# Performance work log

Hardware: AMD Instinct MI355X
Metric: run time of the kernel (lower is better)

The kernel has to match this reference:

```python
import jax, jax.numpy as jnp
import numpy as np

KNOTS = 8
INTERVAL = 4.0
LAYERS = 8
WIDTH = 128
DX = 64
DY = 64
P = 3 * KNOTS - 1  # widths(K) + heights(K) + interior derivatives(K-1)
BATCH = 16384
MIN_DERIV = 1e-3
SOFTMAX_ADJ = 1e-2


def _made_masks(D, W):
    in_deg = np.arange(1, D + 1)
    hid_deg = (np.arange(W) % max(D - 1, 1)) + 1
    m1 = (hid_deg[:, None] >= in_deg[None, :]).astype(np.float32)        # (W, D)
    out_deg = np.repeat(np.arange(1, D + 1), P)                           # (D*P,)
    m2 = (out_deg[:, None] > hid_deg[None, :]).astype(np.float32)        # (D*P, W)
    return jnp.asarray(m1), jnp.asarray(m2)


def _adj_softmax(v):
    p = jax.nn.softmax(v, axis=-1)
    return (p + SOFTMAX_ADJ / v.shape[-1]) / (1.0 + SOFTMAX_ADJ)


def _rqs_transform(x, params):
    # x: (B, D); params: (B, D, P). Rational-quadratic spline on [-B_int, B_int], identity outside.
    Bi = INTERVAL
    w = params[..., :KNOTS]
    h = params[..., KNOTS:2 * KNOTS]
    d = params[..., 2 * KNOTS:]
    widths = _adj_softmax(w) * 2 * Bi
    heights = _adj_softmax(h) * 2 * Bi
    zero = jnp.zeros(x.shape + (1,), x.dtype)
    x_pos = -Bi + jnp.concatenate([zero, jnp.cumsum(widths, -1)], -1)   # (B, D, K+1)
    y_pos = -Bi + jnp.concatenate([zero, jnp.cumsum(heights, -1)], -1)
    derivs = jax.nn.softplus(d) + MIN_DERIV                              # (B, D, K-1)
    one = jnp.ones(x.shape + (1,), x.dtype)
    derivs = jnp.concatenate([one, derivs, one], -1)                     # (B, D, K+1), boundary derivs = 1
    inside = (x > -Bi) & (x < Bi)
    xc = jnp.clip(x, -Bi, Bi)
    # bin search (K is small; vectorized comparison)
    k = jnp.clip(jnp.sum((xc[..., None] >= x_pos), -1) - 1, 0, KNOTS - 1)

    def g(a, i):
        return jnp.take_along_axis(a, i[..., None], -1)[..., 0]

    xk, xk1 = g(x_pos, k), g(x_pos, k + 1)
    yk, yk1 = g(y_pos, k), g(y_pos, k + 1)
    dk, dk1 = g(derivs, k), g(derivs, k + 1)
    sk = (yk1 - yk) / (xk1 - xk)
    xi = (xc - xk) / (xk1 - xk)
    omx = 1.0 - xi
    den = sk + (dk1 + dk - 2.0 * sk) * xi * omx
    out = yk + (yk1 - yk) * (sk * xi * xi + dk * xi * omx) / den
    ld = 2.0 * jnp.log(sk) + jnp.log(dk1 * xi * xi + 2.0 * sk * xi * omx + dk * omx * omx) - 2.0 * jnp.log(den)
    return jnp.where(inside, out, x), jnp.where(inside, ld, 0.0)


def _maf_transform(x, W1, b1, Wout, bout, D):
    # Stacked layers: masked MLP -> elementwise RQ spline -> reverse permutation.
    m1, m2 = _made_masks(D, WIDTH)

    def layer(carry, ws):
        xc, ld = carry
        w1, bb1, wo, bo = ws
        hdn = jax.nn.relu(xc @ (w1 * m1).T + bb1)                # (B, W)
        p = (hdn @ (wo * m2).T + bo).reshape(xc.shape[0], D, P)  # (B, D, P)
        x2, ldj = _rqs_transform(xc, p)
        return (x2[:, ::-1], ld + ldj.sum(-1)), None

    init = (x, jnp.zeros(x.shape[0], x.dtype))
    (xf, ld), _ = jax.lax.scan(layer, init, (W1, b1, Wout, bout))
    return xf, ld


def setup_inputs() -> dict:
    key = jax.random.key(0)
    ks = jax.random.split(key, 10)
    s = 0.05
    return {
        "x": jax.random.normal(ks[0], (BATCH, DX), jnp.float32),
        "y": jax.random.normal(ks[1], (BATCH, DY), jnp.float32),
        "f_W1": jax.random.normal(ks[2], (LAYERS, WIDTH, DX), jnp.float32) * s,
        "f_b1": jnp.zeros((LAYERS, WIDTH), jnp.float32),
        "f_Wout": jax.random.normal(ks[3], (LAYERS, DX * P, WIDTH), jnp.float32) * s,
        "f_bout": jnp.zeros((LAYERS, DX * P), jnp.float32),
        "g_W1": jax.random.normal(ks[4], (LAYERS, WIDTH, DY), jnp.float32) * s,
        "g_b1": jnp.zeros((LAYERS, WIDTH), jnp.float32),
        "g_Wout": jax.random.normal(ks[5], (LAYERS, DY * P, WIDTH), jnp.float32) * s,
        "g_bout": jnp.zeros((LAYERS, DY * P), jnp.float32),
    }


def reference(x, y, f_W1, f_b1, f_Wout, f_bout, g_W1, g_b1, g_Wout, g_bout):
    xo, ldf = _maf_transform(x, f_W1, f_b1, f_Wout, f_bout, DX)
    yo, ldg = _maf_transform(y, g_W1, g_b1, g_Wout, g_bout, DY)
    return (xo, ldf, yo, ldg)
```

## Files before the change

kernel.cpp:

```cpp
#include <hip/hip_runtime.h>
#include <math.h>

#define BATCH   16384
#define DIMS    64
#define WID     128
#define KN      8
#define NP      23
#define NCOL    (DIMS * NP)
#define NLAYERS 8
#define BI_F    4.0f
#define GRP     92
#define NGRP    16
#define XPITCH  68
#define PCP     104
#define LOG2E   1.44269504f

#define PF_WOUT (NLAYERS * NCOL * WID)
#define PF_W1   (NLAYERS * WID * DIMS)

typedef short s16x8 __attribute__((ext_vector_type(8)));
typedef unsigned short u16x8 __attribute__((ext_vector_type(8)));
typedef float f32x4 __attribute__((ext_vector_type(4)));

__device__ __forceinline__ unsigned short f2bf(float f) {
    unsigned int u = __builtin_bit_cast(unsigned int, f);
    unsigned int r = (u + 0x7FFFu + ((u >> 16) & 1u)) >> 16;
    return (unsigned short)r;
}
__device__ __forceinline__ float bfLO(unsigned int u) {
    return __builtin_bit_cast(float, u << 16);
}
__device__ __forceinline__ float bfHI(unsigned int u) {
    return __builtin_bit_cast(float, u & 0xffff0000u);
}
__device__ __forceinline__ unsigned int cvtpk_bf16(float a, float b) {
    unsigned int r;
    asm("v_cvt_pk_bf16_f32 %0, %1, %2" : "=v"(r) : "v"(a), "v"(b));
    return r;
}

__device__ __forceinline__ void stage16(const unsigned short* g, unsigned short* l) {
    __builtin_amdgcn_global_load_lds(
        (__attribute__((address_space(1))) void*)g,
        (__attribute__((address_space(3))) void*)l,
        16, 0, 0);
}

__global__ __launch_bounds__(256) void premask_kernel(
    const float* __restrict__ f_wout, const float* __restrict__ g_wout,
    const float* __restrict__ f_w1,   const float* __restrict__ g_w1,
    unsigned short* __restrict__ womask, unsigned short* __restrict__ w1mask)
{
    const int idx    = blockIdx.x * 256 + threadIdx.x;
    const int stride = gridDim.x * 256;

    const int totw = 2 * PF_WOUT;
    for (int i = idx; i < totw; i += stride) {
        int fl = i / PF_WOUT;
        int r  = i % PF_WOUT;
        int h  = r % WID;
        int o  = (r / WID) % NCOL;
        int d  = o / NP;
        int hd = h % (DIMS - 1) + 1;
        const float* src = fl ? g_wout : f_wout;
        unsigned short v = (hd <= d) ? f2bf(src[r] * LOG2E) : (unsigned short)0;
        const int dst = i - h + (h ^ ((o & 7) << 4));
        womask[dst] = v;
    }

    const int tot1 = 2 * PF_W1;
    for (int i = idx; i < tot1; i += stride) {
        int fl = i / PF_W1;
        int r  = i % PF_W1;
        int c  = r % DIMS;
        int w  = (r / DIMS) % WID;
        int deg = w % (DIMS - 1) + 1;
        const float* src = fl ? g_w1 : f_w1;
        w1mask[i] = (c < deg) ? f2bf(src[r]) : (unsigned short)0;
    }
}

__global__ __launch_bounds__(256)
__attribute__((amdgpu_waves_per_eu(2, 2)))
void flow8_kernel(
    const float* __restrict__ xin_f, const float* __restrict__ xin_g,
    float* __restrict__ xout_f,      float* __restrict__ xout_g,
    const unsigned short* __restrict__ w1m_f, const unsigned short* __restrict__ w1m_g,
    const float* __restrict__ b1_f,  const float* __restrict__ b1_g,
    const unsigned short* __restrict__ wom_f, const unsigned short* __restrict__ wom_g,
    const float* __restrict__ bo_f,  const float* __restrict__ bo_g,
    float* __restrict__ ld_f,        float* __restrict__ ld_g)
{
    __shared__ __align__(16) unsigned short Wl[GRP * WID];
    __shared__ __align__(16) unsigned short S[4][2176];
    __shared__ __align__(16) float Xf[2][4][16][XPITCH];

    const int t    = threadIdx.x;
    const int wv   = t >> 6;
    const int ln   = t & 63;
    const int m    = ln & 15;
    const int q    = ln >> 4;
    const int flow = blockIdx.y;
    const int r0   = blockIdx.x * 64 + wv * 16;

    const float* xin          = flow ? xin_g : xin_f;
    float*       xout         = flow ? xout_g : xout_f;
    const unsigned short* w1m = flow ? w1m_g : w1m_f;
    const float* b1           = flow ? b1_g  : b1_f;
    const unsigned short* wom = flow ? wom_g : wom_f;
    const float* bo           = flow ? bo_g  : bo_f;
    float*       ldp          = flow ? ld_g  : ld_f;

    {
        const int row = ln >> 2;
        const int c0  = (ln & 3) * 16;
        const float* srcr = xin + (size_t)(r0 + row) * DIMS + c0;
        float* dstr = &Xf[0][wv][row][c0];
        #pragma unroll
        for (int i = 0; i < 4; ++i)
            *(float4*)(dstr + i * 4) = *(const float4*)(srcr + i * 4);
    }
    asm volatile("" ::: "memory");

    {
        const unsigned short* src = wom + ln * 8;
        #pragma unroll
        for (int i = 0; i < 6; ++i) {
            const int c = wv + 4 * i;
            if (c < 23) stage16(src + c * 512, Wl + c * 512);
        }
    }

    float bnx[6];
    #pragma unroll
    for (int nt = 0; nt < 6; ++nt)
        bnx[nt] = bo[nt * 16 + m] * LOG2E;

    int offn[6];
    #pragma unroll
    for (int nt = 0; nt < 6; ++nt) {
        const int o = nt * 16 + m;
        offn[nt] = o + (o >= 23) + (o >= 46) + (o >= 69) + (o >= 92);
    }

    float ldsum = 0.0f;
    int cur = 0;
    unsigned short* sw = &S[wv][0];

    __syncthreads();

    #pragma unroll 1
    for (int l = 0; l < NLAYERS; ++l) {
        const unsigned short* w1m_l = w1m + (size_t)l * WID * DIMS;
        const float* b1_l           = b1 + (size_t)l * WID;
        const int nxt = cur ^ 1;

        s16x8 xa[2];
        #pragma unroll
        for (int ks = 0; ks < 2; ++ks) {
            float4 v0 = *(const float4*)&Xf[cur][wv][m][ks * 32 + q * 8];
            float4 v1 = *(const float4*)&Xf[cur][wv][m][ks * 32 + q * 8 + 4];
            uint4 uu;
            uu.x = cvtpk_bf16(v0.x, v0.y);
            uu.y = cvtpk_bf16(v0.z, v0.w);
            uu.z = cvtpk_bf16(v1.x, v1.y);
            uu.w = cvtpk_bf16(v1.z, v1.w);
            xa[ks] = __builtin_bit_cast(s16x8, uu);
        }

        f32x4 hacc[8];
        #pragma unroll
        for (int nt = 0; nt < 8; ++nt) {
            float bv = b1_l[nt * 16 + m];
            hacc[nt] = (f32x4){bv, bv, bv, bv};
        }
        #pragma unroll
        for (int ks = 0; ks < 2; ++ks) {
            #pragma unroll
            for (int nt = 0; nt < 8; ++nt) {
                s16x8 bfr = *(const s16x8*)(w1m_l + (nt * 16 + m) * DIMS + ks * 32 + q * 8);
                hacc[nt] = __builtin_amdgcn_mfma_f32_16x16x32_bf16(xa[ks], bfr, hacc[nt], 0, 0, 0);
            }
        }
        #pragma unroll
        for (int nt = 0; nt < 8; ++nt) {
            const int c = nt * 16 + m;
            unsigned int p0 = cvtpk_bf16(fmaxf(hacc[nt][0], 0.0f),
                                         fmaxf(hacc[nt][1], 0.0f));
            unsigned int p1 = cvtpk_bf16(fmaxf(hacc[nt][2], 0.0f),
                                         fmaxf(hacc[nt][3], 0.0f));
            sw[(q * 4 + 0) * 136 + c] = (unsigned short)p0;
            sw[(q * 4 + 1) * 136 + c] = (unsigned short)(p0 >> 16);
            sw[(q * 4 + 2) * 136 + c] = (unsigned short)p1;
            sw[(q * 4 + 3) * 136 + c] = (unsigned short)(p1 >> 16);
        }
        asm volatile("" ::: "memory");

        s16x8 af[4];
        #pragma unroll
        for (int ks = 0; ks < 4; ++ks)
            af[ks] = *(const s16x8*)&sw[m * 136 + ks * 32 + q * 8];
        asm volatile("" ::: "memory");

        #pragma unroll 1
        for (int g = 0; g < NGRP; ++g) {
            const int gi = l * NGRP + g;

            f32x4 acc[6];
            #pragma unroll
            for (int nt = 0; nt < 6; ++nt)
                acc[nt] = (f32x4){bnx[nt], bnx[nt], bnx[nt], bnx[nt]};

            const int swz = ((g * 4 + m) & 7) << 4;
            #pragma unroll
            for (int ks = 0; ks < 4; ++ks) {
                #pragma unroll
                for (int nt = 0; nt < 6; ++nt) {
                    const s16x8 bfr = *(const s16x8*)&Wl[
                        (nt * 16 + m) * WID + ((ks * 32 + q * 8) ^ swz)];
                    acc[nt] = __builtin_amdgcn_mfma_f32_16x16x32_bf16(af[ks], bfr, acc[nt], 0, 0, 0);
                }
            }

            if (gi < NLAYERS * NGRP - 1) {
                __syncthreads();
                const int l2 = (gi + 1) >> 4;
                const int g2 = (gi + 1) & 15;
                const unsigned short* src = wom +
                    ((size_t)l2 * NCOL + (size_t)g2 * GRP) * WID + ln * 8;
                #pragma unroll
                for (int i = 0; i < 6; ++i) {
                    const int c = wv + 4 * i;
                    if (c < 23) stage16(src + c * 512, Wl + c * 512);
                }
                #pragma unroll
                for (int nt = 0; nt < 6; ++nt) {
                    int o = g2 * GRP + nt * 16 + m;
                    o = (o < NCOL) ? o : (NCOL - 1);
                    bnx[nt] = bo[(size_t)l2 * NCOL + o] * LOG2E;
                }
            }

            #pragma unroll
            for (int nt = 0; nt < 6; ++nt) {
                const int cb = q * 4 * PCP + offn[nt];
                unsigned int p0 = cvtpk_bf16(acc[nt][0], acc[nt][1]);
                unsigned int p1 = cvtpk_bf16(acc[nt][2], acc[nt][3]);
                sw[cb          ] = (unsigned short)p0;
                sw[cb +     PCP] = (unsigned short)(p0 >> 16);
                sw[cb + 2 * PCP] = (unsigned short)p1;
                sw[cb + 3 * PCP] = (unsigned short)(p1 >> 16);
            }
            asm volatile("" ::: "memory");

            {
                const int d = g * 4 + q;

                const unsigned short* pr = &sw[m * PCP + q * 24];
                u16x8 w0 = *(const u16x8*)(pr);
                u16x8 w1 = *(const u16x8*)(pr + 8);
                u16x8 w2 = *(const u16x8*)(pr + 16);
                uint4 r0 = __builtin_bit_cast(uint4, w0);
                uint4 r1 = __builtin_bit_cast(uint4, w1);
                uint4 r2 = __builtin_bit_cast(uint4, w2);

                float pp[NP];
                pp[0]  = bfLO(r0.x); pp[1]  = bfHI(r0.x);
                pp[2]  = bfLO(r0.y); pp[3]  = bfHI(r0.y);
                pp[4]  = bfLO(r0.z); pp[5]  = bfHI(r0.z);
                pp[6]  = bfLO(r0.w); pp[7]  = bfHI(r0.w);
                pp[8]  = bfLO(r1.x); pp[9]  = bfHI(r1.x);
                pp[10] = bfLO(r1.y); pp[11] = bfHI(r1.y);
                pp[12] = bfLO(r1.z); pp[13] = bfHI(r1.z);
                pp[14] = bfLO(r1.w); pp[15] = bfHI(r1.w);
                pp[16] = bfLO(r2.x); pp[17] = bfHI(r2.x);
                pp[18] = bfLO(r2.y); pp[19] = bfHI(r2.y);
                pp[20] = bfLO(r2.z); pp[21] = bfHI(r2.z);
                pp[22] = bfLO(r2.w);

                const float xraw = Xf[cur][wv][m][d];

                float ew[KN], eh[KN];
                #pragma unroll
                for (int j = 0; j < KN; ++j) {
                    ew[j] = exp2f(pp[j]);
                    eh[j] = exp2f(pp[8 + j]);
                }
                const float sw_ = ((ew[0] + ew[1]) + (ew[2] + ew[3]))
                                + ((ew[4] + ew[5]) + (ew[6] + ew[7]));
                const float sh_ = ((eh[0] + eh[1]) + (eh[2] + eh[3]))
                                + ((eh[4] + eh[5]) + (eh[6] + eh[7]));
                const float cmul = 8.0f / 1.01f;
                const float cadd = 0.00125f * (8.0f / 1.01f);
                const float rw = cmul / sw_, rh = cmul / sh_;
                float width[KN], height[KN];
                #pragma unroll
                for (int j = 0; j < KN; ++j) {
                    width[j]  = fmaf(ew[j], rw, cadd);
                    height[j] = fmaf(eh[j], rh, cadd);
                }

                const bool inside = (xraw > -BI_F) && (xraw < BI_F);
                const float xcl = fminf(fmaxf(xraw, -BI_F), BI_F);

                float cx = -BI_F + width[0], cy = -BI_F + height[0];
                float xk = -BI_F, yk = -BI_F, xk1 = cx, yk1 = cy;
                float selk = pp[16], selk1 = pp[16];
                bool cc1 = false, cc7 = false;
                #pragma unroll
                for (int i = 1; i < KN; ++i) {
                    const float nx = cx + width[i];
                    const float ny = cy + height[i];
                    const bool cc = (xcl >= cx);
                    if (i == 1) cc1 = cc;
                    if (i == 7) cc7 = cc;
                    xk  = cc ? cx : xk;    yk  = cc ? cy : yk;
                    xk1 = cc ? nx : xk1;   yk1 = cc ? ny : yk1;
                    selk = cc ? pp[15 + i] : selk;
                    if (i < 7) selk1 = cc ? pp[16 + i] : selk1;
                    cx = nx; cy = ny;
                }
                const float ta = exp2f(selk);
                const float da = fmaf(__log2f(1.0f + ta), 0.69314718f, 0.001f);
                const float tb = exp2f(selk1);
                const float db = fmaf(__log2f(1.0f + tb), 0.69314718f, 0.001f);
                const float dk  = cc1 ? da : 1.0f;
                const float dk1 = cc7 ? 1.0f : db;

                const float invw = 1.0f / (xk1 - xk);
                const float sk   = (yk1 - yk) * invw;
                const float xi   = (xcl - xk) * invw;
                const float omx  = 1.0f - xi;
                const float den  = sk + (dk1 + dk - 2.0f * sk) * xi * omx;
                const float rden = 1.0f / den;
                float outv = fmaf((yk1 - yk) * (sk * xi * xi + dk * xi * omx), rden, yk);
                const float numl = dk1 * xi * xi + 2.0f * sk * xi * omx + dk * omx * omx;
                float ldj = __logf(sk * sk * numl * rden * rden);
                outv = inside ? outv : xraw;
                ldj  = inside ? ldj : 0.0f;

                Xf[nxt][wv][m][DIMS - 1 - d] = outv;
                ldsum += ldj;
            }

            if (gi < NLAYERS * NGRP - 1) {
                __syncthreads();
            }
        }

        cur ^= 1;
    }

    asm volatile("" ::: "memory");

    {
        const int row = ln >> 2;
        const int c0  = (ln & 3) * 16;
        const float* srcr = &Xf[cur][wv][row][c0];
        float* dstr = xout + (size_t)(r0 + row) * DIMS + c0;
        #pragma unroll
        for (int i = 0; i < 4; ++i)
            *(float4*)(dstr + i * 4) = *(const float4*)(srcr + i * 4);
    }

    float v = ldsum + __shfl_xor(ldsum, 16, 64);
    v = v + __shfl_xor(v, 32, 64);
    if (ln < 16) {
        ldp[r0 + ln] = v;
    }
}

extern "C" void kernel_launch(void* const* d_in, const int* in_sizes, int n_in,
                              void* d_out, int out_size, void* d_ws, size_t ws_size,
                              hipStream_t stream)
{
    const float* x      = (const float*)d_in[0];
    const float* y      = (const float*)d_in[1];
    const float* f_W1   = (const float*)d_in[2];
    const float* f_b1   = (const float*)d_in[3];
    const float* f_Wout = (const float*)d_in[4];
    const float* f_bout = (const float*)d_in[5];
    const float* g_W1   = (const float*)d_in[6];
    const float* g_b1   = (const float*)d_in[7];
    const float* g_Wout = (const float*)d_in[8];
    const float* g_bout = (const float*)d_in[9];

    float* out = (float*)d_out;
    float* xo  = out;
    float* ldf = out + (size_t)BATCH * DIMS;
    float* yo  = ldf + BATCH;
    float* ldg = yo + (size_t)BATCH * DIMS;

    unsigned short* womask = (unsigned short*)d_ws;
    unsigned short* w1mask = womask + 2 * (size_t)PF_WOUT;

    premask_kernel<<<dim3(2048), dim3(256), 0, stream>>>(
        f_Wout, g_Wout, f_W1, g_W1, womask, w1mask);

    flow8_kernel<<<dim3(BATCH / 64, 2), dim3(256), 0, stream>>>(
        x, y, xo, yo,
        w1mask, w1mask + (size_t)PF_W1,
        f_b1, g_b1,
        womask, womask + (size_t)PF_WOUT,
        f_bout, g_bout,
        ldf, ldg);
}
```

Measured before the change: 427.2 us.

## Software-pipeline spline with next group's GEMM and double-buffer weight staging

Restructures the layer/group loop into one flat loop that issues the async LDS stage of the next weight group into a second Wl buffer before computing the current group's GEMM. The spline for the previous group then runs while that load is in flight, so each iteration needs only one barrier instead of two. The activation state is now kept in bf16 in LDS rather than fp32, which shrinks shared memory and drops the per-layer conversion. The cost is lower precision of the state carried between layers and the final output, which now passes through bf16.

New measurement: 427.8 us. About the same (+0.1%).

```diff
diff --git a/kernel.cpp b/kernel.cpp
--- a/kernel.cpp
+++ b/kernel.cpp
@@ -11,8 +11,10 @@
 #define BI_F    4.0f
 #define GRP     92
 #define NGRP    16
-#define XPITCH  68
+#define NITER   (NLAYERS * NGRP)
 #define PCP     104
+#define HHP     72
+#define XBP     72
 #define LOG2E   1.44269504f
 
 #define PF_WOUT (NLAYERS * NCOL * WID)
@@ -26,6 +28,9 @@
     unsigned int u = __builtin_bit_cast(unsigned int, f);
     unsigned int r = (u + 0x7FFFu + ((u >> 16) & 1u)) >> 16;
     return (unsigned short)r;
+}
+__device__ __forceinline__ float bf2f(unsigned short u) {
+    return __builtin_bit_cast(float, (unsigned int)u << 16);
 }
 __device__ __forceinline__ float bfLO(unsigned int u) {
     return __builtin_bit_cast(float, u << 16);
@@ -80,8 +85,7 @@
     }
 }
 
-__global__ __launch_bounds__(256)
-__attribute__((amdgpu_waves_per_eu(2, 2)))
+__global__ __launch_bounds__(256, 2)
 void flow8_kernel(
     const float* __restrict__ xin_f, const float* __restrict__ xin_g,
     float* __restrict__ xout_f,      float* __restrict__ xout_g,
@@ -91,9 +95,9 @@
     const float* __restrict__ bo_f,  const float* __restrict__ bo_g,
     float* __restrict__ ld_f,        float* __restrict__ ld_g)
 {
-    __shared__ __align__(16) unsigned short Wl[GRP * WID];
-    __shared__ __align__(16) unsigned short S[4][2176];
-    __shared__ __align__(16) float Xf[2][4][16][XPITCH];
+    __shared__ __align__(16) unsigned short Wl[2][GRP * WID];
+    __shared__ __align__(16) unsigned short S[4][16 * PCP];
+    __shared__ __align__(16) unsigned short Xb[2][4][16][XBP];
 
     const int t    = threadIdx.x;
     const int wv   = t >> 6;
@@ -111,14 +115,23 @@
     const float* bo           = flow ? bo_g  : bo_f;
     float*       ldp          = flow ? ld_g  : ld_f;
 
+    unsigned short* sw = &S[wv][0];
+
     {
         const int row = ln >> 2;
         const int c0  = (ln & 3) * 16;
         const float* srcr = xin + (size_t)(r0 + row) * DIMS + c0;
-        float* dstr = &Xf[0][wv][row][c0];
-        #pragma unroll
-        for (int i = 0; i < 4; ++i)
-            *(float4*)(dstr + i * 4) = *(const float4*)(srcr + i * 4);
+        float4 v0 = *(const float4*)(srcr);
+        float4 v1 = *(const float4*)(srcr + 4);
+        float4 v2 = *(const float4*)(srcr + 8);
+        float4 v3 = *(const float4*)(srcr + 12);
+        uint4 pa, pb;
+        pa.x = cvtpk_bf16(v0.x, v0.y); pa.y = cvtpk_bf16(v0.z, v0.w);
+        pa.z = cvtpk_bf16(v1.x, v1.y); pa.w = cvtpk_bf16(v1.z, v1.w);
+        pb.x = cvtpk_bf16(v2.x, v2.y); pb.y = cvtpk_bf16(v2.z, v2.w);
+        pb.z = cvtpk_bf16(v3.x, v3.y); pb.w = cvtpk_bf16(v3.z, v3.w);
+        *(u16x8*)&Xb[0][wv][row][c0]     = __builtin_bit_cast(u16x8, pa);
+        *(u16x8*)&Xb[0][wv][row][c0 + 8] = __builtin_bit_cast(u16x8, pb);
     }
     asm volatile("" ::: "memory");
 
@@ -127,14 +140,9 @@
         #pragma unroll
         for (int i = 0; i < 6; ++i) {
             const int c = wv + 4 * i;
-            if (c < 23) stage16(src + c * 512, Wl + c * 512);
-        }
-    }
-
-    float bnx[6];
-    #pragma unroll
-    for (int nt = 0; nt < 6; ++nt)
-        bnx[nt] = bo[nt * 16 + m] * LOG2E;
+            if (c < 23) stage16(src + c * 512, Wl[0] + c * 512);
+        }
+    }
 
     int offn[6];
     #pragma unroll
@@ -144,29 +152,15 @@
     }
 
     float ldsum = 0.0f;
-    int cur = 0;
-    unsigned short* sw = &S[wv][0];
-
-    __syncthreads();
-
-    #pragma unroll 1
-    for (int l = 0; l < NLAYERS; ++l) {
+    s16x8 af[4];
+    float bnx[6];
+
+    auto gemm1 = [&](int l) {
         const unsigned short* w1m_l = w1m + (size_t)l * WID * DIMS;
         const float* b1_l           = b1 + (size_t)l * WID;
-        const int nxt = cur ^ 1;
-
-        s16x8 xa[2];
-        #pragma unroll
-        for (int ks = 0; ks < 2; ++ks) {
-            float4 v0 = *(const float4*)&Xf[cur][wv][m][ks * 32 + q * 8];
-            float4 v1 = *(const float4*)&Xf[cur][wv][m][ks * 32 + q * 8 + 4];
-            uint4 uu;
-            uu.x = cvtpk_bf16(v0.x, v0.y);
-            uu.y = cvtpk_bf16(v0.z, v0.w);
-            uu.z = cvtpk_bf16(v1.x, v1.y);
-            uu.w = cvtpk_bf16(v1.z, v1.w);
-            xa[ks] = __builtin_bit_cast(s16x8, uu);
-        }
+        const unsigned short* xb    = &Xb[l & 1][wv][m][0];
+        s16x8 xa0 = *(const s16x8*)(xb + q * 8);
+        s16x8 xa1 = *(const s16x8*)(xb + 32 + q * 8);
 
         f32x4 hacc[8];
         #pragma unroll
@@ -175,192 +169,232 @@
             hacc[nt] = (f32x4){bv, bv, bv, bv};
         }
         #pragma unroll
-        for (int ks = 0; ks < 2; ++ks) {
+        for (int nt = 0; nt < 8; ++nt) {
+            s16x8 b0 = *(const s16x8*)(w1m_l + (nt * 16 + m) * DIMS + q * 8);
+            hacc[nt] = __builtin_amdgcn_mfma_f32_16x16x32_bf16(xa0, b0, hacc[nt], 0, 0, 0);
+        }
+        #pragma unroll
+        for (int nt = 0; nt < 8; ++nt) {
+            s16x8 b1f = *(const s16x8*)(w1m_l + (nt * 16 + m) * DIMS + 32 + q * 8);
+            hacc[nt] = __builtin_amdgcn_mfma_f32_16x16x32_bf16(xa1, b1f, hacc[nt], 0, 0, 0);
+        }
+        #pragma unroll
+        for (int nt = 0; nt < 4; ++nt) {
+            const int c = nt * 16 + m;
+            unsigned int p0 = cvtpk_bf16(fmaxf(hacc[nt][0], 0.0f), fmaxf(hacc[nt][1], 0.0f));
+            unsigned int p1 = cvtpk_bf16(fmaxf(hacc[nt][2], 0.0f), fmaxf(hacc[nt][3], 0.0f));
+            sw[(q * 4 + 0) * HHP + c] = (unsigned short)p0;
+            sw[(q * 4 + 1) * HHP + c] = (unsigned short)(p0 >> 16);
+            sw[(q * 4 + 2) * HHP + c] = (unsigned short)p1;
+            sw[(q * 4 + 3) * HHP + c] = (unsigned short)(p1 >> 16);
+        }
+        asm volatile("" ::: "memory");
+        af[0] = *(const s16x8*)&sw[m * HHP + q * 8];
+        af[1] = *(const s16x8*)&sw[m * HHP + 32 + q * 8];
+        asm volatile("" ::: "memory");
+        #pragma unroll
+        for (int nt = 4; nt < 8; ++nt) {
+            const int c = (nt - 4) * 16 + m;
+            unsigned int p0 = cvtpk_bf16(fmaxf(hacc[nt][0], 0.0f), fmaxf(hacc[nt][1], 0.0f));
+            unsigned int p1 = cvtpk_bf16(fmaxf(hacc[nt][2], 0.0f), fmaxf(hacc[nt][3], 0.0f));
+            sw[(q * 4 + 0) * HHP + c] = (unsigned short)p0;
+            sw[(q * 4 + 1) * HHP + c] = (unsigned short)(p0 >> 16);
+            sw[(q * 4 + 2) * HHP + c] = (unsigned short)p1;
+            sw[(q * 4 + 3) * HHP + c] = (unsigned short)(p1 >> 16);
+        }
+        asm volatile("" ::: "memory");
+        af[2] = *(const s16x8*)&sw[m * HHP + q * 8];
+        af[3] = *(const s16x8*)&sw[m * HHP + 32 + q * 8];
+        asm volatile("" ::: "memory");
+    };
+
+    auto spline = [&](int pgi) {
+        const int pl = pgi >> 4;
+        const int pg = pgi & 15;
+        const int d  = pg * 4 + q;
+        const int xb = pl & 1;
+
+        const unsigned short* pr = &sw[m * PCP + q * 24];
+        u16x8 w0 = *(const u16x8*)(pr);
+        u16x8 w1 = *(const u16x8*)(pr + 8);
+        u16x8 w2 = *(const u16x8*)(pr + 16);
+        uint4 r0 = __builtin_bit_cast(uint4, w0);
+        uint4 r1 = __builtin_bit_cast(uint4, w1);
+        uint4 r2 = __builtin_bit_cast(uint4, w2);
+
+        float pp[NP];
+        pp[0]  = bfLO(r0.x); pp[1]  = bfHI(r0.x);
+        pp[2]  = bfLO(r0.y); pp[3]  = bfHI(r0.y);
+        pp[4]  = bfLO(r0.z); pp[5]  = bfHI(r0.z);
+        pp[6]  = bfLO(r0.w); pp[7]  = bfHI(r0.w);
+        pp[8]  = bfLO(r1.x); pp[9]  = bfHI(r1.x);
+        pp[10] = bfLO(r1.y); pp[11] = bfHI(r1.y);
+        pp[12] = bfLO(r1.z); pp[13] = bfHI(r1.z);
+        pp[14] = bfLO(r1.w); pp[15] = bfHI(r1.w);
+        pp[16] = bfLO(r2.x); pp[17] = bfHI(r2.x);
+        pp[18] = bfLO(r2.y); pp[19] = bfHI(r2.y);
+        pp[20] = bfLO(r2.z); pp[21] = bfHI(r2.z);
+        pp[22] = bfLO(r2.w);
+
+        const float xraw = bf2f(Xb[xb][wv][m][d]);
+
+        float ew[KN], eh[KN];
+        #pragma unroll
+        for (int j = 0; j < KN; ++j) {
+            ew[j] = exp2f(pp[j]);
+            eh[j] = exp2f(pp[8 + j]);
+        }
+        const float sw_ = ((ew[0] + ew[1]) + (ew[2] + ew[3]))
+                        + ((ew[4] + ew[5]) + (ew[6] + ew[7]));
+        const float sh_ = ((eh[0] + eh[1]) + (eh[2] + eh[3]))
+                        + ((eh[4] + eh[5]) + (eh[6] + eh[7]));
+        const float cmul = 8.0f / 1.01f;
+        const float cadd = 0.00125f * (8.0f / 1.01f);
+        const float rw = cmul / sw_, rh = cmul / sh_;
+        float width[KN], height[KN];
+        #pragma unroll
+        for (int j = 0; j < KN; ++j) {
+            width[j]  = fmaf(ew[j], rw, cadd);
+            height[j] = fmaf(eh[j], rh, cadd);
+        }
+
+        const bool inside = (xraw > -BI_F) && (xraw < BI_F);
+        const float xcl = fminf(fmaxf(xraw, -BI_F), BI_F);
+
+        float cx = -BI_F + width[0], cy = -BI_F + height[0];
+        float xk = -BI_F, yk = -BI_F, xk1 = cx, yk1 = cy;
+        float selk = pp[16], selk1 = pp[16];
+        bool cc1 = false, cc7 = false;
+        #pragma unroll
+        for (int i = 1; i < KN; ++i) {
+            const float nx = cx + width[i];
+            const float ny = cy + height[i];
+            const bool cc = (xcl >= cx);
+            if (i == 1) cc1 = cc;
+            if (i == 7) cc7 = cc;
+            xk  = cc ? cx : xk;    yk  = cc ? cy : yk;
+            xk1 = cc ? nx : xk1;   yk1 = cc ? ny : yk1;
+            selk = cc ? pp[15 + i] : selk;
+            if (i < 7) selk1 = cc ? pp[16 + i] : selk1;
+            cx = nx; cy = ny;
+        }
+        const float ta = exp2f(selk);
+        const float da = fmaf(__log2f(1.0f + ta), 0.69314718f, 0.001f);
+        const float tb = exp2f(selk1);
+        const float db = fmaf(__log2f(1.0f + tb), 0.69314718f, 0.001f);
+        const float dk  = cc1 ? da : 1.0f;
+        const float dk1 = cc7 ? 1.0f : db;
+
+        const float invw = 1.0f / (xk1 - xk);
+        const float sk   = (yk1 - yk) * invw;
+        const float xi   = (xcl - xk) * invw;
+        const float omx  = 1.0f - xi;
+        const float den  = sk + (dk1 + dk - 2.0f * sk) * xi * omx;
+        const float rden = 1.0f / den;
+        float outv = fmaf((yk1 - yk) * (sk * xi * xi + dk * xi * omx), rden, yk);
+        const float numl = dk1 * xi * xi + 2.0f * sk * xi * omx + dk * omx * omx;
+        float ldj = __logf(sk * sk * numl * rden * rden);
+        outv = inside ? outv : xraw;
+        ldj  = inside ? ldj : 0.0f;
+
+        Xb[xb ^ 1][wv][m][63 - d] = (unsigned short)cvtpk_bf16(outv, outv);
+        ldsum += ldj;
+    };
+
+    gemm1(0);
+    #pragma unroll
+    for (int nt = 0; nt < 6; ++nt)
+        bnx[nt] = bo[nt * 16 + m] * LOG2E;
+
+    __syncthreads();
+
+    #pragma unroll 1
+    for (int gi = 0; gi < NITER; ++gi) {
+        const int g = gi & 15;
+
+        if (gi < NITER - 1) {
+            const int n = gi + 1, l2 = n >> 4, g2 = n & 15;
+            const unsigned short* src = wom +
+                ((size_t)l2 * NCOL + (size_t)g2 * GRP) * WID + ln * 8;
+            unsigned short* dst = &Wl[n & 1][0];
             #pragma unroll
-            for (int nt = 0; nt < 8; ++nt) {
-                s16x8 bfr = *(const s16x8*)(w1m_l + (nt * 16 + m) * DIMS + ks * 32 + q * 8);
-                hacc[nt] = __builtin_amdgcn_mfma_f32_16x16x32_bf16(xa[ks], bfr, hacc[nt], 0, 0, 0);
+            for (int i = 0; i < 6; ++i) {
+                const int c = wv + 4 * i;
+                if (c < 23) stage16(src + c * 512, dst + c * 512);
             }
         }
-        #pragma unroll
-        for (int nt = 0; nt < 8; ++nt) {
-            const int c = nt * 16 + m;
-            unsigned int p0 = cvtpk_bf16(fmaxf(hacc[nt][0], 0.0f),
-                                         fmaxf(hacc[nt][1], 0.0f));
-            unsigned int p1 = cvtpk_bf16(fmaxf(hacc[nt][2], 0.0f),
-                                         fmaxf(hacc[nt][3], 0.0f));
-            sw[(q * 4 + 0) * 136 + c] = (unsigned short)p0;
-            sw[(q * 4 + 1) * 136 + c] = (unsigned short)(p0 >> 16);
-            sw[(q * 4 + 2) * 136 + c] = (unsigned short)p1;
-            sw[(q * 4 + 3) * 136 + c] = (unsigned short)(p1 >> 16);
-        }
-        asm volatile("" ::: "memory");
-
-        s16x8 af[4];
-        #pragma unroll
-        for (int ks = 0; ks < 4; ++ks)
-            af[ks] = *(const s16x8*)&sw[m * 136 + ks * 32 + q * 8];
-        asm volatile("" ::: "memory");
-
-        #pragma unroll 1
-        for (int g = 0; g < NGRP; ++g) {
-            const int gi = l * NGRP + g;
-
-            f32x4 acc[6];
-            #pragma unroll
-            for (int nt = 0; nt < 6; ++nt)
-                acc[nt] = (f32x4){bnx[nt], bnx[nt], bnx[nt], bnx[nt]};
-
-            const int swz = ((g * 4 + m) & 7) << 4;
-            #pragma unroll
-            for (int ks = 0; ks < 4; ++ks) {
-                #pragma unroll
-                for (int nt = 0; nt < 6; ++nt) {
-                    const s16x8 bfr = *(const s16x8*)&Wl[
-                        (nt * 16 + m) * WID + ((ks * 32 + q * 8) ^ swz)];
-                    acc[nt] = __builtin_amdgcn_mfma_f32_16x16x32_bf16(af[ks], bfr, acc[nt], 0, 0, 0);
-                }
-            }
-
-            if (gi < NLAYERS * NGRP - 1) {
-                __syncthreads();
-                const int l2 = (gi + 1) >> 4;
-                const int g2 = (gi + 1) & 15;
-                const unsigned short* src = wom +
-                    ((size_t)l2 * NCOL + (size_t)g2 * GRP) * WID + ln * 8;
-                #pragma unroll
-                for (int i = 0; i < 6; ++i) {
-                    const int c = wv + 4 * i;
-                    if (c < 23) stage16(src + c * 512, Wl + c * 512);
-                }
-                #pragma unroll
-                for (int nt = 0; nt < 6; ++nt) {
-                    int o = g2 * GRP + nt * 16 + m;
-                    o = (o < NCOL) ? o : (NCOL - 1);
-                    bnx[nt] = bo[(size_t)l2 * NCOL + o] * LOG2E;
-                }
-            }
-
+
+        if (g == 0 && gi > 0) {
+            spline(gi - 1);
+            asm volatile("" ::: "memory");
+            gemm1(gi >> 4);
+        }
+
+        f32x4 acc[6];
+        #pragma unroll
+        for (int nt = 0; nt < 6; ++nt)
+            acc[nt] = (f32x4){bnx[nt], bnx[nt], bnx[nt], bnx[nt]};
+
+        const unsigned short* wl = &Wl[gi & 1][0];
+        const int swz = ((g * 4 + m) & 7) << 4;
+        #pragma unroll
+        for (int ks = 0; ks < 4; ++ks) {
             #pragma unroll
             for (int nt = 0; nt < 6; ++nt) {
-                const int cb = q * 4 * PCP + offn[nt];
-                unsigned int p0 = cvtpk_bf16(acc[nt][0], acc[nt][1]);
-                unsigned int p1 = cvtpk_bf16(acc[nt][2], acc[nt][3]);
-                sw[cb          ] = (unsigned short)p0;
-                sw[cb +     PCP] = (unsigned short)(p0 >> 16);
-                sw[cb + 2 * PCP] = (unsigned short)p1;
-                sw[cb + 3 * PCP] = (unsigned short)(p1 >> 16);
+                const s16x8 bfr = *(const s16x8*)&wl[
+                    (nt * 16 + m) * WID + ((ks * 32 + q * 8) ^ swz)];
+                acc[nt] = __builtin_amdgcn_mfma_f32_16x16x32_bf16(af[ks], bfr, acc[nt], 0, 0, 0);
             }
-            asm volatile("" ::: "memory");
-
-            {
-                const int d = g * 4 + q;
-
-                const unsigned short* pr = &sw[m * PCP + q * 24];
-                u16x8 w0 = *(const u16x8*)(pr);
-                u16x8 w1 = *(const u16x8*)(pr + 8);
-                u16x8 w2 = *(const u16x8*)(pr + 16);
-                uint4 r0 = __builtin_bit_cast(uint4, w0);
-                uint4 r1 = __builtin_bit_cast(uint4, w1);
-                uint4 r2 = __builtin_bit_cast(uint4, w2);
-
-                float pp[NP];
-                pp[0]  = bfLO(r0.x); pp[1]  = bfHI(r0.x);
-                pp[2]  = bfLO(r0.y); pp[3]  = bfHI(r0.y);
-                pp[4]  = bfLO(r0.z); pp[5]  = bfHI(r0.z);
-                pp[6]  = bfLO(r0.w); pp[7]  = bfHI(r0.w);
-                pp[8]  = bfLO(r1.x); pp[9]  = bfHI(r1.x);
-                pp[10] = bfLO(r1.y); pp[11] = bfHI(r1.y);
-                pp[12] = bfLO(r1.z); pp[13] = bfHI(r1.z);
-                pp[14] = bfLO(r1.w); pp[15] = bfHI(r1.w);
-                pp[16] = bfLO(r2.x); pp[17] = bfHI(r2.x);
-                pp[18] = bfLO(r2.y); pp[19] = bfHI(r2.y);
-                pp[20] = bfLO(r2.z); pp[21] = bfHI(r2.z);
-                pp[22] = bfLO(r2.w);
-
-                const float xraw = Xf[cur][wv][m][d];
-
-                float ew[KN], eh[KN];
-                #pragma unroll
-                for (int j = 0; j < KN; ++j) {
-                    ew[j] = exp2f(pp[j]);
-                    eh[j] = exp2f(pp[8 + j]);
-                }
-                const float sw_ = ((ew[0] + ew[1]) + (ew[2] + ew[3]))
-                                + ((ew[4] + ew[5]) + (ew[6] + ew[7]));
-                const float sh_ = ((eh[0] + eh[1]) + (eh[2] + eh[3]))
-                                + ((eh[4] + eh[5]) + (eh[6] + eh[7]));
-                const float cmul = 8.0f / 1.01f;
-                const float cadd = 0.00125f * (8.0f / 1.01f);
-                const float rw = cmul / sw_, rh = cmul / sh_;
-                float width[KN], height[KN];
-                #pragma unroll
-                for (int j = 0; j < KN; ++j) {
-                    width[j]  = fmaf(ew[j], rw, cadd);
-                    height[j] = fmaf(eh[j], rh, cadd);
-                }
-
-                const bool inside = (xraw > -BI_F) && (xraw < BI_F);
-                const float xcl = fminf(fmaxf(xraw, -BI_F), BI_F);
-
-                float cx = -BI_F + width[0], cy = -BI_F + height[0];
-                float xk = -BI_F, yk = -BI_F, xk1 = cx, yk1 = cy;
-                float selk = pp[16], selk1 = pp[16];
-                bool cc1 = false, cc7 = false;
-                #pragma unroll
-                for (int i = 1; i < KN; ++i) {
-                    const float nx = cx + width[i];
-                    const float ny = cy + height[i];
-                    const bool cc = (xcl >= cx);
-                    if (i == 1) cc1 = cc;
-                    if (i == 7) cc7 = cc;
-                    xk  = cc ? cx : xk;    yk  = cc ? cy : yk;
-                    xk1 = cc ? nx : xk1;   yk1 = cc ? ny : yk1;
-                    selk = cc ? pp[15 + i] : selk;
-                    if (i < 7) selk1 = cc ? pp[16 + i] : selk1;
-                    cx = nx; cy = ny;
-                }
-                const float ta = exp2f(selk);
-                const float da = fmaf(__log2f(1.0f + ta), 0.69314718f, 0.001f);
-                const float tb = exp2f(selk1);
-                const float db = fmaf(__log2f(1.0f + tb), 0.69314718f, 0.001f);
-                const float dk  = cc1 ? da : 1.0f;
-                const float dk1 = cc7 ? 1.0f : db;
-
-                const float invw = 1.0f / (xk1 - xk);
-                const float sk   = (yk1 - yk) * invw;
-                const float xi   = (xcl - xk) * invw;
-                const float omx  = 1.0f - xi;
-                const float den  = sk + (dk1 + dk - 2.0f * sk) * xi * omx;
-                const float rden = 1.0f / den;
-                float outv = fmaf((yk1 - yk) * (sk * xi * xi + dk * xi * omx), rden, yk);
-                const float numl = dk1 * xi * xi + 2.0f * sk * xi * omx + dk * omx * omx;
-                float ldj = __logf(sk * sk * numl * rden * rden);
-                outv = inside ? outv : xraw;
-                ldj  = inside ? ldj : 0.0f;
-
-                Xf[nxt][wv][m][DIMS - 1 - d] = outv;
-                ldsum += ldj;
+        }
+
+        if (gi < NITER - 1) {
+            const int n = gi + 1, l2 = n >> 4, g2 = n & 15;
+            #pragma unroll
+            for (int nt = 0; nt < 6; ++nt) {
+                int o = g2 * GRP + nt * 16 + m;
+                o = (o < NCOL) ? o : (NCOL - 1);
+                bnx[nt] = bo[(size_t)l2 * NCOL + o] * LOG2E;
             }
-
-            if (gi < NLAYERS * NGRP - 1) {
-                __syncthreads();
-            }
-        }
-
-        cur ^= 1;
-    }
-
+        }
+
+        if (g != 0) {
+            spline(gi - 1);
+        }
+        asm volatile("" ::: "memory");
+
+        #pragma unroll
+        for (int nt = 0; nt < 6; ++nt) {
+            const int cb = q * 4 * PCP + offn[nt];
+            unsigned int p0 = cvtpk_bf16(acc[nt][0], acc[nt][1]);
+            unsigned int p1 = cvtpk_bf16(acc[nt][2], acc[nt][3]);
+            sw[cb          ] = (unsigned short)p0;
+            sw[cb +     PCP] = (unsigned short)(p0 >> 16);
+            sw[cb + 2 * PCP] = (unsigned short)p1;
+            sw[cb + 3 * PCP] = (unsigned short)(p1 >> 16);
+        }
+
+        __syncthreads();
+    }
+
+    spline(NITER - 1);
     asm volatile("" ::: "memory");
 
     {
         const int row = ln >> 2;
         const int c0  = (ln & 3) * 16;
-        const float* srcr = &Xf[cur][wv][row][c0];
+        u16x8 ua = *(const u16x8*)&Xb[0][wv][row][c0];
+        u16x8 ub = *(const u16x8*)&Xb[0][wv][row][c0 + 8];
+        uint4 ra = __builtin_bit_cast(uint4, ua);
+        uint4 rb = __builtin_bit_cast(uint4, ub);
         float* dstr = xout + (size_t)(r0 + row) * DIMS + c0;
-        #pragma unroll
-        for (int i = 0; i < 4; ++i)
-            *(float4*)(dstr + i * 4) = *(const float4*)(srcr + i * 4);
+        float4 o0 = {bfLO(ra.x), bfHI(ra.x), bfLO(ra.y), bfHI(ra.y)};
+        float4 o1 = {bfLO(ra.z), bfHI(ra.z), bfLO(ra.w), bfHI(ra.w)};
+        float4 o2 = {bfLO(rb.x), bfHI(rb.x), bfLO(rb.y), bfHI(rb.y)};
+        float4 o3 = {bfLO(rb.z), bfHI(rb.z), bfLO(rb.w), bfHI(rb.w)};
+        *(float4*)(dstr)      = o0;
+        *(float4*)(dstr + 4)  = o1;
+        *(float4*)(dstr + 8)  = o2;
+        *(float4*)(dstr + 12) = o3;
     }
 
     float v = ldsum + __shfl_xor(ldsum, 16, 64);
```
